# Performance work log

Measured on AMD Instinct MI355X. Metric: run time of the kernel, lower is better.

## Reference

```python
import jax, jax.numpy as jnp
import numpy as np

B, S, D_IN, D_Q, D_V, H = 2, 2048, 1024, 1024, 1024, 16
HD_Q, HD_V = D_Q // H, D_V // H
SCALE = float(D_Q) ** 0.5  # source scales by sqrt(d_q), NOT sqrt(head_dim)


def setup_inputs() -> dict:
    key = jax.random.key(0)
    k1, k2, k3, k4, k5 = jax.random.split(key, 5)
    return {
        "x": jax.random.normal(k1, (B, S, D_IN), dtype=jnp.float32),
        "w_q": jax.random.normal(k2, (D_IN, D_Q), dtype=jnp.float32),
        "w_k": jax.random.normal(k3, (D_IN, D_Q), dtype=jnp.float32),
        "w_v": jax.random.normal(k4, (D_IN, D_V), dtype=jnp.float32),
        "W_o": jax.random.normal(k5, (D_IN, D_V), dtype=jnp.float32),
    }


def reference(x, w_q, w_k, w_v, W_o):
    b, s, _ = x.shape
    # projections: [b, s, d]
    q = x @ w_q
    k = x @ w_k
    v = x @ w_v
    # split heads -> [b, h, s, hd]
    Q = q.reshape(b, s, H, HD_Q).transpose(0, 2, 1, 3)
    K = k.reshape(b, s, H, HD_Q).transpose(0, 2, 1, 3)
    V = v.reshape(b, s, H, HD_V).transpose(0, 2, 1, 3)
    # full [b, h, s, s] score matrix (naive attention, as in source)
    scores = jnp.einsum("bhqd,bhkd->bhqk", Q, K)
    # FAITHFUL QUIRK: source applies softmax over dim=0 (batch axis)
    attn = jax.nn.softmax(scores / SCALE, axis=0)
    vals = jnp.einsum("bhqk,bhkd->bhqd", attn, V)
    vals = vals.transpose(0, 2, 1, 3).reshape(b, s, D_V)
    return vals @ W_o
```

## Files before the change

kernel.cpp:

```cpp
#include <hip/hip_runtime.h>


typedef _Float16 f16;
typedef __attribute__((ext_vector_type(8))) _Float16 f16x8;
typedef __attribute__((ext_vector_type(4))) _Float16 f16x4;
typedef __attribute__((ext_vector_type(4))) float f32x4;

#define MFMA16(a,b,c) __builtin_amdgcn_mfma_f32_16x16x32_f16(a,b,c,0,0,0)
#define GLD16(gp, lp) __builtin_amdgcn_global_load_lds(                         \
    (const __attribute__((address_space(1))) void*)(gp),                        \
    (__attribute__((address_space(3))) void*)(lp), 16, 0, 0)

__global__ __launch_bounds__(256) void prep(const float* __restrict__ x,
                                            const float* __restrict__ w0, const float* __restrict__ w1,
                                            const float* __restrict__ w2, const float* __restrict__ w3,
                                            f16* __restrict__ xh,
                                            f16* __restrict__ o0, f16* __restrict__ o1,
                                            f16* __restrict__ o2, f16* __restrict__ o3) {
    const int bb = blockIdx.x;
    const int tid = threadIdx.x;
    if (bb >= 1024) {
        int i = (bb - 1024) * 256 + tid;
        float4 v = ((const float4*)x)[i];
        f16x4 h;
        h[0] = (f16)v.x; h[1] = (f16)v.y; h[2] = (f16)v.z; h[3] = (f16)v.w;
        *(f16x4*)(xh + (long)i * 4) = h;
        return;
    }
    const float* w; f16* o;
    switch (bb & 3) {
        case 0: w = w0; o = o0; break;
        case 1: w = w1; o = o1; break;
        case 2: w = w2; o = o2; break;
        default: w = w3; o = o3; break;
    }
    __shared__ alignas(16) f16 t[64][72];
    const int d0 = ((bb >> 2) & 15) * 64, j0 = (bb >> 6) * 64;
    #pragma unroll
    for (int it = 0; it < 4; ++it) {
        int idx = it * 256 + tid;
        int row = idx >> 4, c4 = idx & 15;
        float4 v = *(const float4*)(w + (long)(d0 + row) * 1024 + j0 + c4 * 4);
        f16x4 h;
        h[0] = (f16)v.x; h[1] = (f16)v.y; h[2] = (f16)v.z; h[3] = (f16)v.w;
        *(f16x4*)&t[row][c4 * 4] = h;
    }
    __syncthreads();
    #pragma unroll
    for (int it = 0; it < 4; ++it) {
        int idx = it * 256 + tid;
        int jr = idx >> 4, d4 = idx & 15;
        f16x4 h;
        #pragma unroll
        for (int m = 0; m < 4; ++m) h[m] = t[d4 * 4 + m][jr];
        *(f16x4*)(o + (long)(j0 + jr) * 1024 + d0 + d4 * 4) = h;
    }
}

__global__ __launch_bounds__(256, 1) void gemm_qkv(const f16* __restrict__ A,
                                                   const f16* __restrict__ Wt,
                                                   f16* __restrict__ Qg,
                                                   f16* __restrict__ Kg,
                                                   f16* __restrict__ Vtg) {
    __shared__ alignas(16) f16 smem[16384];
    f16* As = smem;
    f16* Bs = smem + 8192;
    const int tid = threadIdx.x;
    const int wave = tid >> 6, lane = tid & 63;
    const int l15 = lane & 15, lq = lane >> 4;
    const int sw = l15 & 7;
    const int m0 = blockIdx.x * 128, n0 = blockIdx.y * 128;
    const int wr = (wave >> 1) * 64, wc = (wave & 1) * 64;
    const int r8 = lane >> 3;
    const int swc8 = ((lane & 7) ^ r8) * 8;

    f32x4 acc[4][4] = {};

    for (int kt = 0; kt < 16; ++kt) {
        __syncthreads();
        #pragma unroll
        for (int i = 0; i < 4; ++i) {
            GLD16(A  + (long)(m0 + wave * 32 + i * 8 + r8) * 1024 + kt * 64 + swc8, As + (wave * 32 + i * 8) * 64);
            GLD16(Wt + (long)(n0 + wave * 32 + i * 8 + r8) * 1024 + kt * 64 + swc8, Bs + (wave * 32 + i * 8) * 64);
        }
        __syncthreads();
        #pragma unroll
        for (int s2 = 0; s2 < 2; ++s2) {
            const int rc = ((s2 * 4 + lq) ^ sw) << 3;
            f16x8 af[4], bf[4];
            #pragma unroll
            for (int i = 0; i < 4; ++i) af[i] = *(const f16x8*)&As[(wr + i * 16 + l15) * 64 + rc];
            #pragma unroll
            for (int j = 0; j < 4; ++j) bf[j] = *(const f16x8*)&Bs[(wc + j * 16 + l15) * 64 + rc];
            #pragma unroll
            for (int i = 0; i < 4; ++i)
                #pragma unroll
                for (int j = 0; j < 4; ++j)
                    acc[i][j] = MFMA16(af[i], bf[j], acc[i][j]);
        }
    }

    const int sel = n0 >> 10;
    const int nb = n0 - (sel << 10);

    if (sel < 2) {
        f16* dst = sel == 0 ? Qg : Kg;
        const float qs = sel == 0 ? 0.045084219f : 1.0f;
        __syncthreads();
        #pragma unroll
        for (int i = 0; i < 4; ++i)
            #pragma unroll
            for (int j = 0; j < 4; ++j) {
                int row0 = wr + i * 16 + lq * 4;
                int colb = wc + j * 16 + l15;
                int chunk = colb >> 3, sub = colb & 7;
                #pragma unroll
                for (int r = 0; r < 4; ++r) {
                    int row = row0 + r;
                    smem[row * 128 + ((chunk ^ (row & 7)) << 3) + sub] = (f16)(acc[i][j][r] * qs);
                }
            }
        __syncthreads();
        #pragma unroll
        for (int e = 0; e < 8; ++e) {
            int id = e * 256 + tid;
            int row = id >> 4, c = id & 15;
            f16x8 v = *(const f16x8*)&smem[row * 128 + ((c ^ (row & 7)) << 3)];
            int gr = m0 + row, b = gr >> 11, s = gr & 2047;
            int gc = nb + c * 8, hh = gc >> 6, hd = gc & 63;
            *(f16x8*)(dst + (long)((b * 16 + hh) * 2048 + s) * 64 + hd) = v;
        }
    } else {
        #pragma unroll
        for (int i = 0; i < 4; ++i)
            #pragma unroll
            for (int j = 0; j < 4; ++j) {
                int gr0 = m0 + wr + i * 16 + lq * 4;
                int gc  = nb + wc + j * 16 + l15;
                int b = gr0 >> 11, s = gr0 & 2047;
                int hh = gc >> 6, hd = gc & 63;
                f16x4 v;
                #pragma unroll
                for (int r = 0; r < 4; ++r) v[r] = (f16)acc[i][j][r];
                *(f16x4*)(Vtg + (long)((b * 16 + hh) * 64 + hd) * 2048 + s) = v;
            }
    }
}

template<int NSUM>
__global__ __launch_bounds__(256, 1) void gemm_out(const f16* __restrict__ A0,
                                                   const f16* __restrict__ A1,
                                                   const f16* __restrict__ A2,
                                                   const f16* __restrict__ A3,
                                                   const f16* __restrict__ Bt,
                                                   float* __restrict__ outp) {
    __shared__ alignas(16) f16 As[64][72];
    __shared__ alignas(16) f16 Bs[128][64];
    const int tid = threadIdx.x;
    const int wave = tid >> 6, lane = tid & 63;
    const int l15 = lane & 15, lq = lane >> 4;
    const int sw = l15 & 7;
    const int m0 = blockIdx.x * 64, n0 = blockIdx.y * 128;
    const int wr = (wave >> 1) * 32, wc = (wave & 1) * 64;
    const int r8 = lane >> 3;
    const int swc8 = ((lane & 7) ^ r8) * 8;

    f32x4 acc[2][4] = {};

    for (int kt = 0; kt < 16; ++kt) {
        __syncthreads();
        #pragma unroll
        for (int it = 0; it < 2; ++it) {
            int idx = it * 256 + tid;
            int row = idx >> 3, c = idx & 7;
            long off = (long)(m0 + row) * 1024 + kt * 64 + c * 8;
            f16x8 a = *(const f16x8*)(A0 + off) + *(const f16x8*)(A1 + off);
            if constexpr (NSUM == 4)
                a = a + *(const f16x8*)(A2 + off) + *(const f16x8*)(A3 + off);
            *(f16x8*)&As[row][c * 8] = a;
        }
        #pragma unroll
        for (int i = 0; i < 4; ++i)
            GLD16(Bt + (long)(n0 + wave * 32 + i * 8 + r8) * 1024 + kt * 64 + swc8, &Bs[wave * 32 + i * 8][0]);
        __syncthreads();
        #pragma unroll
        for (int s2 = 0; s2 < 2; ++s2) {
            const int rc = ((s2 * 4 + lq) ^ sw) << 3;
            f16x8 af[2], bf[4];
            #pragma unroll
            for (int i = 0; i < 2; ++i) af[i] = *(const f16x8*)&As[wr + i * 16 + l15][s2 * 32 + lq * 8];
            #pragma unroll
            for (int j = 0; j < 4; ++j) bf[j] = *(const f16x8*)&Bs[wc + j * 16 + l15][rc];
            #pragma unroll
            for (int i = 0; i < 2; ++i)
                #pragma unroll
                for (int j = 0; j < 4; ++j)
                    acc[i][j] = MFMA16(af[i], bf[j], acc[i][j]);
        }
    }

    #pragma unroll
    for (int i = 0; i < 2; ++i)
        #pragma unroll
        for (int j = 0; j < 4; ++j) {
            int gr0 = m0 + wr + i * 16 + lq * 4;
            int gc  = n0 + wc + j * 16 + l15;
            #pragma unroll
            for (int r = 0; r < 4; ++r)
                outp[(long)(gr0 + r) * 1024 + gc] = acc[i][j][r];
        }
}

__global__ __launch_bounds__(256, 3) void attention_kernel(const f16* __restrict__ Qg,
                                                           const f16* __restrict__ Kg,
                                                           const f16* __restrict__ Vtg,
                                                           f16* __restrict__ v0,
                                                           f16* __restrict__ v1,
                                                           f16* __restrict__ v2,
                                                           f16* __restrict__ v3) {
    __shared__ alignas(16) f16 Ks [2][2][32][64];
    __shared__ alignas(16) f16 Vts[2][2][64][32];
    __shared__ alignas(16) f16 Ps [4][2][32][40];
    const int tid = threadIdx.x;
    const int wave = tid >> 6, lane = tid & 63;
    const int l15 = lane & 15, lq = lane >> 4;
    const int sw  = l15 & 7;

    const int NS = gridDim.x >> 8;
    const int nt = 64 / NS;
    const int bid = blockIdx.x;
    const int xcd = bid & 7, sl = bid >> 3;
    const int h  = xcd * 2 + (sl & 1);
    const int qt = (sl >> 1) & 15, ks = sl >> 5;
    const int q0 = qt * 128;
    const int key0 = ks * (nt << 5);
    f16* vals = ks == 0 ? v0 : ks == 1 ? v1 : ks == 2 ? v2 : v3;
    const int qr = q0 + wave * 32;

    f16x8 qfr[2][2][2];
    #pragma unroll
    for (int b2 = 0; b2 < 2; ++b2)
        #pragma unroll
        for (int qq = 0; qq < 2; ++qq)
            #pragma unroll
            for (int s2 = 0; s2 < 2; ++s2)
                qfr[b2][qq][s2] = *(const f16x8*)(Qg + (long)((b2 * 16 + h) * 2048 + qr + qq * 16 + l15) * 64
                                                  + s2 * 32 + lq * 8);

    f32x4 acc[2][2][4] = {};

    const int tb = wave & 1;
    const int r8 = lane >> 3;
    const int swc8 = ((lane & 7) ^ r8) * 8;
    const f16* kbase = Kg  + (long)((tb * 16 + h) * 2048 + key0) * 64 + r8 * 64 + swc8;
    const f16* vbase = Vtg + (long)((tb * 16 + h) * 64 + (lane >> 2)) * 2048 + key0 + (lane & 3) * 8;

    auto stage = [&](int kt, int buf) {
        if (wave < 2) {
            const f16* g = kbase + kt * 2048;
            f16* l = &Ks[buf][tb][0][0];
            #pragma unroll
            for (int i = 0; i < 4; ++i) GLD16(g + i * 512, l + i * 512);
        } else {
            const f16* g = vbase + kt * 32;
            f16* l = &Vts[buf][tb][0][0];
            #pragma unroll
            for (int i = 0; i < 4; ++i) GLD16(g + (long)i * 16 * 2048, l + i * 512);
        }
    };

    stage(0, 0);
    for (int kt = 0; kt < nt; ++kt) {
        const int cur = kt & 1;
        __syncthreads();
        if (kt < nt - 1) stage(kt + 1, cur ^ 1);

        #pragma unroll
        for (int kf = 0; kf < 2; ++kf) {
            f32x4 S0[2] = {}, S1[2] = {};
            __builtin_amdgcn_s_setprio(1);
            #pragma unroll
            for (int s2 = 0; s2 < 2; ++s2) {
                const int rc = ((s2 * 4 + lq) ^ sw) << 3;
                f16x8 a0 = *(const f16x8*)&Ks[cur][0][kf * 16 + l15][rc];
                f16x8 a1 = *(const f16x8*)&Ks[cur][1][kf * 16 + l15][rc];
                #pragma unroll
                for (int qq = 0; qq < 2; ++qq) {
                    S0[qq] = MFMA16(a0, qfr[0][qq][s2], S0[qq]);
                    S1[qq] = MFMA16(a1, qfr[1][qq][s2], S1[qq]);
                }
            }
            __builtin_amdgcn_s_setprio(0);
            #pragma unroll
            for (int qq = 0; qq < 2; ++qq) {
                f16x4 p0v, p1v;
                #pragma unroll
                for (int r = 0; r < 4; ++r) {
                    float e = __builtin_amdgcn_exp2f(S1[qq][r] - S0[qq][r]);
                    float p = __builtin_amdgcn_rcpf(1.0f + e);
                    p0v[r] = (f16)p;
                    p1v[r] = (f16)(1.0f - p);
                }
                const int prow = qq * 16 + l15, pcol = kf * 16 + lq * 4;
                *(f16x4*)&Ps[wave][0][prow][pcol] = p0v;
                *(f16x4*)&Ps[wave][1][prow][pcol] = p1v;
            }
        }

        #pragma unroll
        for (int pb = 0; pb < 2; ++pb) {
            f16x8 pf[2], vf[4];
            #pragma unroll
            for (int qq = 0; qq < 2; ++qq)
                pf[qq] = *(const f16x8*)&Ps[wave][pb][qq * 16 + l15][lq * 8];
            #pragma unroll
            for (int hf = 0; hf < 4; ++hf)
                vf[hf] = *(const f16x8*)&Vts[cur][pb][hf * 16 + l15][lq * 8];
            __builtin_amdgcn_s_setprio(1);
            #pragma unroll
            for (int qq = 0; qq < 2; ++qq)
                #pragma unroll
                for (int hf = 0; hf < 4; ++hf)
                    acc[pb][qq][hf] = MFMA16(pf[qq], vf[hf], acc[pb][qq][hf]);
            __builtin_amdgcn_s_setprio(0);
        }
    }

    #pragma unroll
    for (int b2 = 0; b2 < 2; ++b2)
        #pragma unroll
        for (int qq = 0; qq < 2; ++qq)
            #pragma unroll
            for (int hf = 0; hf < 4; ++hf)
                #pragma unroll
                for (int r = 0; r < 4; ++r)
                    vals[(long)(b2 * 2048 + qr + qq * 16 + lq * 4 + r) * 1024 + h * 64 + hf * 16 + l15]
                        = (f16)acc[b2][qq][hf][r];
}

extern "C" void kernel_launch(void* const* d_in, const int* in_sizes, int n_in,
                              void* d_out, int out_size, void* d_ws, size_t ws_size,
                              hipStream_t stream) {
    const float* x  = (const float*)d_in[0];
    const float* wq = (const float*)d_in[1];
    const float* wk = (const float*)d_in[2];
    const float* wv = (const float*)d_in[3];
    const float* wo = (const float*)d_in[4];

    char* ws = (char*)d_ws;
    f16* xh    = (f16*)(ws);
    f16* wqT   = (f16*)(ws + 8388608);
    f16* wkT   = (f16*)(ws + 10485760);
    f16* wvT   = (f16*)(ws + 12582912);
    f16* woT   = (f16*)(ws + 14680064);
    f16* Qg    = (f16*)(ws + 16777216);
    f16* Kg    = (f16*)(ws + 25165824);
    f16* Vtg   = (f16*)(ws + 33554432);
    f16* vals1 = (f16*)(ws + 41943040);
    f16* vals2 = (f16*)(ws + 50331648);
    f16* vals3 = (f16*)(ws + 58720256);
    f16* vals0 = xh;
    (void)in_sizes; (void)n_in; (void)out_size;

    const int NS = (ws_size >= (size_t)67108864) ? 4 : 2;

    prep<<<5120, 256, 0, stream>>>(x, wq, wk, wv, wo, xh, wqT, wkT, wvT, woT);

    gemm_qkv<<<dim3(32, 24), 256, 0, stream>>>(xh, wqT, Qg, Kg, Vtg);

    attention_kernel<<<NS * 256, 256, 0, stream>>>(Qg, Kg, Vtg, vals0, vals1, vals2, vals3);

    if (NS == 4)
        gemm_out<4><<<dim3(64, 8), 256, 0, stream>>>(vals0, vals1, vals2, vals3, woT, (float*)d_out);
    else
        gemm_out<2><<<dim3(64, 8), 256, 0, stream>>>(vals0, vals1, vals0, vals0, woT, (float*)d_out);
}
```

Baseline: 193.1 us.

## Keep softmax probabilities in registers for PV MFMA, removing LDS round-trip

Instead of writing the probability tile to shared memory and reading it back as MFMA operands, the kernel keeps P in registers and feeds it straight into 16x16x16 MFMAs as the B operand. V becomes the A operand, which transposes the accumulator so output stores become vectorized f16x4 writes. V staging gets an XOR swizzle so the new fragment reads avoid bank conflicts. The cost is twice as many, smaller-K MFMA instructions and more register pressure.

```diff
diff --git a/kernel.cpp b/kernel.cpp
--- a/kernel.cpp
+++ b/kernel.cpp
@@ -6,7 +6,8 @@
 typedef __attribute__((ext_vector_type(4))) _Float16 f16x4;
 typedef __attribute__((ext_vector_type(4))) float f32x4;
 
-#define MFMA16(a,b,c) __builtin_amdgcn_mfma_f32_16x16x32_f16(a,b,c,0,0,0)
+#define MFMA16(a,b,c)  __builtin_amdgcn_mfma_f32_16x16x32_f16(a,b,c,0,0,0)
+#define MFMA16K(a,b,c) __builtin_amdgcn_mfma_f32_16x16x16f16(a,b,c,0,0,0)
 #define GLD16(gp, lp) __builtin_amdgcn_global_load_lds(                         \
     (const __attribute__((address_space(1))) void*)(gp),                        \
     (__attribute__((address_space(3))) void*)(lp), 16, 0, 0)
@@ -220,7 +221,6 @@
                                                            f16* __restrict__ v3) {
     __shared__ alignas(16) f16 Ks [2][2][32][64];
     __shared__ alignas(16) f16 Vts[2][2][64][32];
-    __shared__ alignas(16) f16 Ps [4][2][32][40];
     const int tid = threadIdx.x;
     const int wave = tid >> 6, lane = tid & 63;
     const int l15 = lane & 15, lq = lane >> 4;
@@ -253,7 +253,8 @@
     const int r8 = lane >> 3;
     const int swc8 = ((lane & 7) ^ r8) * 8;
     const f16* kbase = Kg  + (long)((tb * 16 + h) * 2048 + key0) * 64 + r8 * 64 + swc8;
-    const f16* vbase = Vtg + (long)((tb * 16 + h) * 64 + (lane >> 2)) * 2048 + key0 + (lane & 3) * 8;
+    const f16* vbase = Vtg + (long)((tb * 16 + h) * 64 + (lane >> 2)) * 2048 + key0
+                       + ((lane & 3) ^ ((lane >> 2) & 3)) * 8;
 
     auto stage = [&](int kt, int buf) {
         if (wave < 2) {
@@ -269,12 +270,16 @@
         }
     };
 
+    const int vro = l15 * 32 + (lq & 1) * 4 + ((((lq >> 1) ^ (l15 & 3))) << 3);
+    const f16* VtsF = &Vts[0][0][0][0];
+
     stage(0, 0);
     for (int kt = 0; kt < nt; ++kt) {
         const int cur = kt & 1;
         __syncthreads();
         if (kt < nt - 1) stage(kt + 1, cur ^ 1);
 
+        f16x4 pp0[2][2], pp1[2][2];
         #pragma unroll
         for (int kf = 0; kf < 2; ++kf) {
             f32x4 S0[2] = {}, S1[2] = {};
@@ -293,49 +298,53 @@
             __builtin_amdgcn_s_setprio(0);
             #pragma unroll
             for (int qq = 0; qq < 2; ++qq) {
-                f16x4 p0v, p1v;
+                f16x4 p0v;
                 #pragma unroll
                 for (int r = 0; r < 4; ++r) {
                     float e = __builtin_amdgcn_exp2f(S1[qq][r] - S0[qq][r]);
                     float p = __builtin_amdgcn_rcpf(1.0f + e);
                     p0v[r] = (f16)p;
-                    p1v[r] = (f16)(1.0f - p);
                 }
-                const int prow = qq * 16 + l15, pcol = kf * 16 + lq * 4;
-                *(f16x4*)&Ps[wave][0][prow][pcol] = p0v;
-                *(f16x4*)&Ps[wave][1][prow][pcol] = p1v;
+                f16x4 onev = {(f16)1.f, (f16)1.f, (f16)1.f, (f16)1.f};
+                pp0[kf][qq] = p0v;
+                pp1[kf][qq] = onev - p0v;
             }
         }
 
         #pragma unroll
         for (int pb = 0; pb < 2; ++pb) {
-            f16x8 pf[2], vf[4];
-            #pragma unroll
-            for (int qq = 0; qq < 2; ++qq)
-                pf[qq] = *(const f16x8*)&Ps[wave][pb][qq * 16 + l15][lq * 8];
-            #pragma unroll
-            for (int hf = 0; hf < 4; ++hf)
-                vf[hf] = *(const f16x8*)&Vts[cur][pb][hf * 16 + l15][lq * 8];
-            __builtin_amdgcn_s_setprio(1);
-            #pragma unroll
-            for (int qq = 0; qq < 2; ++qq)
+            #pragma unroll
+            for (int kf = 0; kf < 2; ++kf) {
+                f16x4 vfrag[4];
                 #pragma unroll
                 for (int hf = 0; hf < 4; ++hf)
-                    acc[pb][qq][hf] = MFMA16(pf[qq], vf[hf], acc[pb][qq][hf]);
-            __builtin_amdgcn_s_setprio(0);
-        }
-    }
-
-    #pragma unroll
-    for (int b2 = 0; b2 < 2; ++b2)
+                    vfrag[hf] = *(const f16x4*)&VtsF[cur * 4096 + pb * 2048 + hf * 512
+                                                     + (vro ^ (kf << 4))];
+                __builtin_amdgcn_s_setprio(1);
+                #pragma unroll
+                for (int qq = 0; qq < 2; ++qq)
+                    #pragma unroll
+                    for (int hf = 0; hf < 4; ++hf)
+                        acc[pb][qq][hf] = MFMA16K(vfrag[hf],
+                                                  pb ? pp1[kf][qq] : pp0[kf][qq],
+                                                  acc[pb][qq][hf]);
+                __builtin_amdgcn_s_setprio(0);
+            }
+        }
+    }
+
+    #pragma unroll
+    for (int pb = 0; pb < 2; ++pb)
         #pragma unroll
         for (int qq = 0; qq < 2; ++qq)
             #pragma unroll
-            for (int hf = 0; hf < 4; ++hf)
-                #pragma unroll
-                for (int r = 0; r < 4; ++r)
-                    vals[(long)(b2 * 2048 + qr + qq * 16 + lq * 4 + r) * 1024 + h * 64 + hf * 16 + l15]
-                        = (f16)acc[b2][qq][hf][r];
+            for (int hf = 0; hf < 4; ++hf) {
+                f16x4 ov;
+                #pragma unroll
+                for (int r = 0; r < 4; ++r) ov[r] = (f16)acc[pb][qq][hf][r];
+                *(f16x4*)(vals + (long)(pb * 2048 + qr + qq * 16 + l15) * 1024
+                          + h * 64 + hf * 16 + lq * 4) = ov;
+            }
 }
 
 extern "C" void kernel_launch(void* const* d_in, const int* in_sizes, int n_in,
```

Result: slower. 201.1 us (+4.2%).
